# Optimization experiments

Hardware: AMD Instinct MI355X
Metric: run time of the kernel (lower is better)

## Reference

```python
import jax, jax.numpy as jnp
import numpy as np

B = 8192      # batch
D = 512       # ode state dim = 4*h_dim
U = 100       # ode net hidden units
K_STEPS = 20  # opt.ode1_step
EPS = 0.01    # opt.ode2_eps


def setup_inputs() -> dict:
    key = jax.random.key(0)
    ks = jax.random.split(key, 12)
    std = 0.1  # init_network_weights std
    return {
        "y0": jax.random.normal(ks[0], (B, D), jnp.float32),
        "t_seq": jax.random.uniform(ks[1], (B, 2), dtype=jnp.float32),
        "W1": std * jax.random.normal(ks[2], (U, D), jnp.float32),
        "b1": jnp.zeros((U,), jnp.float32),
        "W2": std * jax.random.normal(ks[3], (U, U), jnp.float32),
        "b2": jnp.zeros((U,), jnp.float32),
        "W3": std * jax.random.normal(ks[4], (D, U), jnp.float32),
        "b3": jnp.zeros((D,), jnp.float32),
        "b_phi_zt": jax.random.normal(ks[5], (B, 1), jnp.float32),
        # derivative of Nonpositive net is <= 0; log(-b' + 0.01) requires b' < 0.01
        "b_phi_zt_deriv": -jax.random.uniform(ks[6], (B, 1), dtype=jnp.float32),
        "s_phi_zt": jax.random.normal(ks[7], (B, 1), jnp.float32),
        "s_phi_zt_deriv": jax.random.uniform(ks[8], (B, 1), dtype=jnp.float32),
        "k": K_STEPS,
    }


def _ode_net(y, W1, b1, W2, b2, W3, b3):
    # create_net(D, D, n_layers=1, n_units=U): Linear->Tanh->Linear->Tanh->Linear
    h = jnp.tanh(y @ W1.T + b1)
    h = jnp.tanh(h @ W2.T + b2)
    return h @ W3.T + b3


def _forward(y0, t_seq, W1, b1, W2, b2, W3, b3,
             b_phi_zt, b_phi_zt_deriv, s_phi_zt, s_phi_zt_deriv, k):
    # ---- DiffeqSolver: k fixed Euler steps, gradient net ignores t ----
    dt = (t_seq[:, 1:2] - t_seq[:, 0:1]) / k  # [B,1]

    def euler_step(yi, _):
        yi = yi + _ode_net(yi, W1, b1, W2, b2, W3, b3) * dt
        return yi, None

    y_final, _ = jax.lax.scan(euler_step, y0, None, length=k)

    # ---- DiffeqSolver_KL: y_t = y0 + eps * cumsum(g(m_t)); y0 = 0 ----
    const = 0.01
    Kv = s_phi_zt + jnp.log(-b_phi_zt_deriv + const) - jnp.log(s_phi_zt_deriv + const)  # [B,1]
    T = int(round(1.0 / EPS)) - 1  # steps t = 1 .. int(1/eps)-1
    ms = (-1.0 + EPS * jnp.arange(1, T + 1, dtype=jnp.float32))[:, None, None]  # [T,1,1]
    log_neg_m = jnp.log(-ms)
    gm = -b_phi_zt_deriv / (ms * log_neg_m) * (Kv - jnp.log(-log_neg_m))  # [T,B,1]
    ycum = EPS * jnp.cumsum(gm, axis=0)  # solutions[t-1] = ycum[t-1]
    loss = ycum[-1] + (ycum[-2] - ycum[-1])  # first_item + Gm_eps  -> [B,1]

    return jnp.concatenate([y_final, loss], axis=-1)  # [B, D+1]


def reference(y0, t_seq, W1, b1, W2, b2, W3, b3,
              b_phi_zt, b_phi_zt_deriv, s_phi_zt, s_phi_zt_deriv, k):
    return _forward(y0, t_seq, W1, b1, W2, b2, W3, b3,
                    b_phi_zt, b_phi_zt_deriv, s_phi_zt, s_phi_zt_deriv, k)
```

## Files before the change

### kernel.cpp

```cpp
#include <hip/hip_runtime.h>


typedef __attribute__((ext_vector_type(8))) short s16x8;
typedef __attribute__((ext_vector_type(4))) float fx4;

#define NB   8192
#define DD   512
#define UU   100
#define UP   128
#define BM   32

__device__ __forceinline__ unsigned int f2bf(float x) {
  unsigned int u = __float_as_uint(x);
  return (u + 0x7FFFu + ((u >> 16) & 1u)) >> 16;
}
__device__ __forceinline__ float bf2f(unsigned int h) {
  return __uint_as_float(h << 16);
}
__device__ __forceinline__ float tanh_fast(float x) {
  float e = __expf(2.0f * x);
  return 1.0f - 2.0f / (e + 1.0f);
}

__global__ void prep_weights(const float* __restrict__ W1,
                             const float* __restrict__ W2,
                             const float* __restrict__ W3,
                             unsigned short* __restrict__ ws) {
  int e = blockIdx.x * 256 + threadIdx.x;
  if (e < 65536) {
    int u = e >> 9, kc = e & 511;
    ws[e] = (u < UU) ? (unsigned short)f2bf(W1[u * DD + kc]) : (unsigned short)0;
  } else if (e < 81920) {
    int e2 = e - 65536;
    int n = e2 >> 7, kc = e2 & 127;
    ws[e] = (n < UU && kc < UU) ? (unsigned short)f2bf(W2[n * UU + kc]) : (unsigned short)0;
  } else if (e < 147456) {
    int e3 = e - 81920;
    int d = e3 >> 7, kc = e3 & 127;
    ws[e] = (kc < UU) ? (unsigned short)f2bf(W3[d * UU + kc]) : (unsigned short)0;
  }
}

__global__ __launch_bounds__(512) __attribute__((amdgpu_waves_per_eu(2, 2)))
void ode_main(
    const float* __restrict__ y0, const float* __restrict__ t_seq,
    const float* __restrict__ b1, const float* __restrict__ b2,
    const float* __restrict__ b3,
    const unsigned short* __restrict__ W1b,
    const unsigned short* __restrict__ W2b,
    const unsigned short* __restrict__ W3b,
    const int* __restrict__ kptr, float* __restrict__ out) {
  __shared__ char Yb[BM * DD * 2];
  __shared__ char H1s[BM * UP * 2];
  __shared__ char H2s[BM * UP * 2];
  __shared__ char W2s[UP * UP * 2];

  const int tid  = threadIdx.x;
  const int w    = tid >> 6;
  const int lane = tid & 63;
  const int lo   = lane & 15;
  const int hi   = lane >> 4;
  const int m2   = w >> 2;
  const int n0   = 2 * (w & 3);
  const int b0   = blockIdx.x * BM;
  const int k    = *kptr;
  const float kinv = 1.0f / (float)k;

  auto yboff = [](int b, int byr) -> int { return (b << 10) + (byr ^ ((b & 7) << 4)); };
  auto hoff  = [](int r, int byr) -> int { return (r << 8)  + (byr ^ ((r & 7) << 4)); };

  s16x8 w1r[16];
#pragma unroll
  for (int kk = 0; kk < 16; ++kk)
    w1r[kk] = *(const s16x8*)(W1b + (16 * w + lo) * DD + kk * 32 + hi * 8);
  s16x8 w3r[4][4];
#pragma unroll
  for (int i = 0; i < 4; ++i)
#pragma unroll
    for (int kk = 0; kk < 4; ++kk)
      w3r[i][kk] = *(const s16x8*)(W3b + ((4 * w + i) * 16 + lo) * UP + kk * 32 + hi * 8);

  for (int g = tid; g < 2048; g += 512) {
    int n = g >> 4, c8 = g & 15;
    uint4 v = *(const uint4*)(W2b + n * UP + c8 * 8);
    *(uint4*)(W2s + (n << 8) + ((c8 * 16) ^ ((n & 7) << 4))) = v;
  }

  float b1v[4];
#pragma unroll
  for (int r = 0; r < 4; ++r) {
    int u = 16 * w + 4 * hi + r;
    b1v[r] = (u < UU) ? b1[u] : 0.0f;
  }
  float b2v[2];
#pragma unroll
  for (int nj = 0; nj < 2; ++nj) {
    int u = (n0 + nj) * 16 + lo;
    b2v[nj] = (u < UU) ? b2[u] : 0.0f;
  }
  float dtrow[4];
#pragma unroll
  for (int r = 0; r < 4; ++r) {
    int b = b0 + m2 * 16 + 4 * hi + r;
    dtrow[r] = (t_seq[2 * b + 1] - t_seq[2 * b]) * kinv;
  }
  float dt3[2];
#pragma unroll
  for (int j = 0; j < 2; ++j) {
    int b = b0 + j * 16 + lo;
    dt3[j] = (t_seq[2 * b + 1] - t_seq[2 * b]) * kinv;
  }
  float b3v[4][4];
#pragma unroll
  for (int i = 0; i < 4; ++i)
#pragma unroll
    for (int r = 0; r < 4; ++r)
      b3v[i][r] = b3[(4 * w + i) * 16 + 4 * hi + r];

  fx4 Yr[4][2];
#pragma unroll
  for (int i = 0; i < 4; ++i)
#pragma unroll
    for (int j = 0; j < 2; ++j) {
      const float* p = y0 + (size_t)(b0 + j * 16 + lo) * DD + (4 * w + i) * 16 + 4 * hi;
      Yr[i][j] = *(const fx4*)p;
    }

  auto write_yb = [&]() {
#pragma unroll
    for (int i = 0; i < 4; ++i)
#pragma unroll
      for (int j = 0; j < 2; ++j) {
        int b   = j * 16 + lo;
        int byr = ((4 * w + i) * 16 + 4 * hi) * 2;
        uint2 q;
        q.x = f2bf(Yr[i][j][0]) | (f2bf(Yr[i][j][1]) << 16);
        q.y = f2bf(Yr[i][j][2]) | (f2bf(Yr[i][j][3]) << 16);
        *(uint2*)(Yb + yboff(b, byr)) = q;
      }
  };
  write_yb();
  __syncthreads();

  const fx4 zf = {0.f, 0.f, 0.f, 0.f};

#pragma unroll 1
  for (int s = 0; s < k; ++s) {
    fx4 acc1[2];
    acc1[0] = zf; acc1[1] = zf;
#pragma unroll
    for (int kk = 0; kk < 16; ++kk) {
      int bro = kk * 64 + hi * 16;
      s16x8 bb0 = *(const s16x8*)(Yb + yboff(lo, bro));
      s16x8 bb1 = *(const s16x8*)(Yb + yboff(16 + lo, bro));
      acc1[0] = __builtin_amdgcn_mfma_f32_16x16x32_bf16(w1r[kk], bb0, acc1[0], 0, 0, 0);
      acc1[1] = __builtin_amdgcn_mfma_f32_16x16x32_bf16(w1r[kk], bb1, acc1[1], 0, 0, 0);
    }
#pragma unroll
    for (int j = 0; j < 2; ++j) {
      int b   = j * 16 + lo;
      int byr = (16 * w + 4 * hi) * 2;
      uint2 q;
      q.x = f2bf(tanh_fast(acc1[j][0] + b1v[0])) |
            (f2bf(tanh_fast(acc1[j][1] + b1v[1])) << 16);
      q.y = f2bf(tanh_fast(acc1[j][2] + b1v[2])) |
            (f2bf(tanh_fast(acc1[j][3] + b1v[3])) << 16);
      *(uint2*)(H1s + hoff(b, byr)) = q;
    }
    __syncthreads();

    fx4 acc2[2];
    acc2[0] = zf; acc2[1] = zf;
#pragma unroll
    for (int kk = 0; kk < 4; ++kk) {
      int bro = kk * 64 + hi * 16;
      s16x8 am  = *(const s16x8*)(H1s + hoff(m2 * 16 + lo, bro));
      s16x8 wb0 = *(const s16x8*)(W2s + hoff((n0 + 0) * 16 + lo, bro));
      s16x8 wb1 = *(const s16x8*)(W2s + hoff((n0 + 1) * 16 + lo, bro));
      acc2[0] = __builtin_amdgcn_mfma_f32_16x16x32_bf16(am, wb0, acc2[0], 0, 0, 0);
      acc2[1] = __builtin_amdgcn_mfma_f32_16x16x32_bf16(am, wb1, acc2[1], 0, 0, 0);
    }
#pragma unroll
    for (int nj = 0; nj < 2; ++nj) {
      int byr = ((n0 + nj) * 16 + lo) * 2;
#pragma unroll
      for (int r = 0; r < 4; ++r) {
        int b = m2 * 16 + 4 * hi + r;
        float hv = tanh_fast(acc2[nj][r] + b2v[nj]) * dtrow[r];
        *(unsigned short*)(H2s + hoff(b, byr)) = (unsigned short)f2bf(hv);
      }
    }
    __syncthreads();

#pragma unroll
    for (int kk = 0; kk < 4; ++kk) {
      int bro = kk * 64 + hi * 16;
      s16x8 bb0 = *(const s16x8*)(H2s + hoff(lo, bro));
      s16x8 bb1 = *(const s16x8*)(H2s + hoff(16 + lo, bro));
#pragma unroll
      for (int i = 0; i < 4; ++i) {
        Yr[i][0] = __builtin_amdgcn_mfma_f32_16x16x32_bf16(w3r[i][kk], bb0, Yr[i][0], 0, 0, 0);
        Yr[i][1] = __builtin_amdgcn_mfma_f32_16x16x32_bf16(w3r[i][kk], bb1, Yr[i][1], 0, 0, 0);
      }
    }
#pragma unroll
    for (int i = 0; i < 4; ++i)
#pragma unroll
      for (int j = 0; j < 2; ++j)
#pragma unroll
        for (int r = 0; r < 4; ++r) Yr[i][j][r] += b3v[i][r] * dt3[j];

    write_yb();
    __syncthreads();
  }

  for (int idx = tid; idx < BM * DD; idx += 512) {
    int b = idx >> 9, d = idx & 511;
    unsigned short h = *(const unsigned short*)(Yb + yboff(b, 2 * d));
    out[(size_t)(b0 + b) * 513 + d] = bf2f((unsigned int)h);
  }
}

__global__ void loss_kernel(const float* __restrict__ bdp,
                            const float* __restrict__ sp,
                            const float* __restrict__ sdp,
                            float* __restrict__ out) {
  int b = blockIdx.x * 256 + threadIdx.x;
  if (b >= NB) return;
  float bd = bdp[b];
  float Kv = sp[b] + __logf(-bd + 0.01f) - __logf(sdp[b] + 0.01f);
  float acc = 0.0f;
  for (int t = 1; t <= 98; ++t) {
    float m = 0.01f * (float)t - 1.0f;
    float L = __logf(-m);
    acc += (-bd) / (m * L) * (Kv - __logf(-L));
  }
  out[(size_t)b * 513 + 512] = 0.01f * acc;
}

extern "C" void kernel_launch(void* const* d_in, const int* in_sizes, int n_in,
                              void* d_out, int out_size, void* d_ws, size_t ws_size,
                              hipStream_t stream) {
  const float* y0    = (const float*)d_in[0];
  const float* t_seq = (const float*)d_in[1];
  const float* W1    = (const float*)d_in[2];
  const float* b1    = (const float*)d_in[3];
  const float* W2    = (const float*)d_in[4];
  const float* b2    = (const float*)d_in[5];
  const float* W3    = (const float*)d_in[6];
  const float* b3    = (const float*)d_in[7];
  const float* bd    = (const float*)d_in[9];
  const float* s_    = (const float*)d_in[10];
  const float* sd    = (const float*)d_in[11];
  const int*   kptr  = (const int*)d_in[12];
  float* out = (float*)d_out;
  unsigned short* ws = (unsigned short*)d_ws;

  prep_weights<<<576, 256, 0, stream>>>(W1, W2, W3, ws);
  ode_main<<<256, 512, 0, stream>>>(y0, t_seq, b1, b2, b3,
                                    ws, ws + 65536, ws + 81920, kptr, out);
  loss_kernel<<<32, 256, 0, stream>>>(bd, s_, sd, out);
}
```

Baseline: 110.8 us.

## Use hardware bf16 pack, exp2 tanh, split accumulators and setprio around MFMAs

Replaces the software round-to-nearest bf16 conversion with the v_cvt_pk_bf16_f32 instruction and computes tanh via exp2 with a prescaled argument. The layer-1 MFMA chain is split into two independent accumulators so consecutive MFMAs do not depend on each other, and s_setprio raises wave priority around the MFMA phases. The aim is to cut VALU work in the epilogues and shorten the MFMA dependency chain. Precision and NaN handling of the hardware convert may differ slightly from the manual rounding.

Result: faster. 102.3 us (-7.7%).

```diff
diff --git a/kernel.cpp b/kernel.cpp
--- a/kernel.cpp
+++ b/kernel.cpp
@@ -17,8 +17,13 @@
 __device__ __forceinline__ float bf2f(unsigned int h) {
   return __uint_as_float(h << 16);
 }
-__device__ __forceinline__ float tanh_fast(float x) {
-  float e = __expf(2.0f * x);
+__device__ __forceinline__ unsigned int cvt_pk_bf16(float lo, float hi) {
+  unsigned int r;
+  asm("v_cvt_pk_bf16_f32 %0, %1, %2" : "=v"(r) : "v"(lo), "v"(hi));
+  return r;
+}
+__device__ __forceinline__ float tanh5(float x) {
+  float e = __builtin_amdgcn_exp2f(x * 2.885390081777927f);
   return 1.0f - 2.0f / (e + 1.0f);
 }
 
@@ -134,8 +139,8 @@
         int b   = j * 16 + lo;
         int byr = ((4 * w + i) * 16 + 4 * hi) * 2;
         uint2 q;
-        q.x = f2bf(Yr[i][j][0]) | (f2bf(Yr[i][j][1]) << 16);
-        q.y = f2bf(Yr[i][j][2]) | (f2bf(Yr[i][j][3]) << 16);
+        q.x = cvt_pk_bf16(Yr[i][j][0], Yr[i][j][1]);
+        q.y = cvt_pk_bf16(Yr[i][j][2], Yr[i][j][3]);
         *(uint2*)(Yb + yboff(b, byr)) = q;
       }
   };
@@ -146,31 +151,41 @@
 
 #pragma unroll 1
   for (int s = 0; s < k; ++s) {
-    fx4 acc1[2];
-    acc1[0] = zf; acc1[1] = zf;
-#pragma unroll
-    for (int kk = 0; kk < 16; ++kk) {
-      int bro = kk * 64 + hi * 16;
-      s16x8 bb0 = *(const s16x8*)(Yb + yboff(lo, bro));
-      s16x8 bb1 = *(const s16x8*)(Yb + yboff(16 + lo, bro));
-      acc1[0] = __builtin_amdgcn_mfma_f32_16x16x32_bf16(w1r[kk], bb0, acc1[0], 0, 0, 0);
-      acc1[1] = __builtin_amdgcn_mfma_f32_16x16x32_bf16(w1r[kk], bb1, acc1[1], 0, 0, 0);
-    }
+    fx4 aA[2], aB[2];
+    aA[0] = zf; aA[1] = zf; aB[0] = zf; aB[1] = zf;
+    __builtin_amdgcn_s_setprio(1);
+#pragma unroll
+    for (int kk = 0; kk < 16; kk += 2) {
+      int bro0 = kk * 64 + hi * 16;
+      int bro1 = (kk + 1) * 64 + hi * 16;
+      s16x8 b00 = *(const s16x8*)(Yb + yboff(lo, bro0));
+      s16x8 b01 = *(const s16x8*)(Yb + yboff(16 + lo, bro0));
+      s16x8 b10 = *(const s16x8*)(Yb + yboff(lo, bro1));
+      s16x8 b11 = *(const s16x8*)(Yb + yboff(16 + lo, bro1));
+      aA[0] = __builtin_amdgcn_mfma_f32_16x16x32_bf16(w1r[kk], b00, aA[0], 0, 0, 0);
+      aA[1] = __builtin_amdgcn_mfma_f32_16x16x32_bf16(w1r[kk], b01, aA[1], 0, 0, 0);
+      aB[0] = __builtin_amdgcn_mfma_f32_16x16x32_bf16(w1r[kk + 1], b10, aB[0], 0, 0, 0);
+      aB[1] = __builtin_amdgcn_mfma_f32_16x16x32_bf16(w1r[kk + 1], b11, aB[1], 0, 0, 0);
+    }
+    __builtin_amdgcn_s_setprio(0);
 #pragma unroll
     for (int j = 0; j < 2; ++j) {
       int b   = j * 16 + lo;
       int byr = (16 * w + 4 * hi) * 2;
+      float v0 = aA[j][0] + aB[j][0] + b1v[0];
+      float v1 = aA[j][1] + aB[j][1] + b1v[1];
+      float v2 = aA[j][2] + aB[j][2] + b1v[2];
+      float v3 = aA[j][3] + aB[j][3] + b1v[3];
       uint2 q;
-      q.x = f2bf(tanh_fast(acc1[j][0] + b1v[0])) |
-            (f2bf(tanh_fast(acc1[j][1] + b1v[1])) << 16);
-      q.y = f2bf(tanh_fast(acc1[j][2] + b1v[2])) |
-            (f2bf(tanh_fast(acc1[j][3] + b1v[3])) << 16);
+      q.x = cvt_pk_bf16(tanh5(v0), tanh5(v1));
+      q.y = cvt_pk_bf16(tanh5(v2), tanh5(v3));
       *(uint2*)(H1s + hoff(b, byr)) = q;
     }
     __syncthreads();
 
     fx4 acc2[2];
     acc2[0] = zf; acc2[1] = zf;
+    __builtin_amdgcn_s_setprio(1);
 #pragma unroll
     for (int kk = 0; kk < 4; ++kk) {
       int bro = kk * 64 + hi * 16;
@@ -180,18 +195,21 @@
       acc2[0] = __builtin_amdgcn_mfma_f32_16x16x32_bf16(am, wb0, acc2[0], 0, 0, 0);
       acc2[1] = __builtin_amdgcn_mfma_f32_16x16x32_bf16(am, wb1, acc2[1], 0, 0, 0);
     }
+    __builtin_amdgcn_s_setprio(0);
 #pragma unroll
     for (int nj = 0; nj < 2; ++nj) {
       int byr = ((n0 + nj) * 16 + lo) * 2;
 #pragma unroll
       for (int r = 0; r < 4; ++r) {
         int b = m2 * 16 + 4 * hi + r;
-        float hv = tanh_fast(acc2[nj][r] + b2v[nj]) * dtrow[r];
-        *(unsigned short*)(H2s + hoff(b, byr)) = (unsigned short)f2bf(hv);
+        float hv = tanh5(acc2[nj][r] + b2v[nj]) * dtrow[r];
+        unsigned int pk = cvt_pk_bf16(hv, hv);
+        *(unsigned short*)(H2s + hoff(b, byr)) = (unsigned short)pk;
       }
     }
     __syncthreads();
 
+    __builtin_amdgcn_s_setprio(1);
 #pragma unroll
     for (int kk = 0; kk < 4; ++kk) {
       int bro = kk * 64 + hi * 16;
@@ -203,6 +221,7 @@
         Yr[i][1] = __builtin_amdgcn_mfma_f32_16x16x32_bf16(w3r[i][kk], bb1, Yr[i][1], 0, 0, 0);
       }
     }
+    __builtin_amdgcn_s_setprio(0);
 #pragma unroll
     for (int i = 0; i < 4; ++i)
 #pragma unroll
```
